# Performance work log

Hardware: AMD Instinct MI355X
Metric: run time of the kernel (lower is better)

## Reference

```python
import jax, jax.numpy as jnp
import numpy as np


def _conv(x, w, b, stride=1, pad=0):
    # x: NCHW, w: OIHW (torch layout)
    y = jax.lax.conv_general_dilated(
        x, w, (stride, stride), [(pad, pad), (pad, pad)],
        dimension_numbers=('NCHW', 'OIHW', 'NCHW'))
    return y + b[None, :, None, None]


def _convT(x, w, b):
    # torch ConvTranspose2d(k=4, stride=2, padding=1); w: [Cin, Cout, 4, 4]
    wf = jnp.flip(w, (2, 3)).transpose(1, 0, 2, 3)  # -> OIHW
    y = jax.lax.conv_general_dilated(
        x, wf, (1, 1), [(2, 2), (2, 2)], lhs_dilation=(2, 2),
        dimension_numbers=('NCHW', 'OIHW', 'NCHW'))
    return y + b[None, :, None, None]


def _quantize(z, embed):
    # z: [B,H,W,D], embed: [D,K]  (eval-mode _Quantize: no EMA update)
    f = z.reshape(-1, z.shape[-1])
    dist = (f * f).sum(1, keepdims=True) - 2.0 * (f @ embed) + (embed * embed).sum(0, keepdims=True)
    ind = jnp.argmin(dist, axis=1)
    q = embed.T[ind].reshape(z.shape)
    diff = jnp.mean((jax.lax.stop_gradient(q) - z) ** 2)[None]
    q = z + jax.lax.stop_gradient(q - z)  # straight-through
    return q, diff, ind.reshape(z.shape[:-1])


def setup_inputs() -> dict:
    key = jax.random.key(0)
    ks = jax.random.split(key, 22)
    s = 0.02
    r = lambda k, sh, sc=s: jax.random.normal(k, sh, jnp.float32) * sc
    z = lambda sh: jnp.zeros(sh, jnp.float32)
    return {
        'x': jax.random.normal(ks[0], (16, 3, 256, 256), jnp.float32),
        # encoder_bottom: two stride-2 4x4 convs, 3->128->128 (256->64)
        'wb1': r(ks[1], (128, 3, 4, 4)), 'bb1': z(128),
        'wb2': r(ks[2], (128, 128, 4, 4)), 'bb2': z(128),
        # encoder_top: one stride-2 4x4 conv, 128->128 (64->32)
        'wt1': r(ks[3], (128, 128, 4, 4)), 'bt1': z(128),
        # quantize_conv_t: 1x1, 128->64
        'wqt': r(ks[4], (64, 128, 1, 1)), 'bqt': z(64),
        'embed_t': jax.random.normal(ks[5], (64, 512), jnp.float32),
        # decoder_top: convT 64->64 (32->64)
        'wdt': r(ks[6], (64, 64, 4, 4)), 'bdt': z(64),
        # quantize_conv_b: 1x1, 192->64
        'wqb': r(ks[7], (64, 192, 1, 1)), 'bqb': z(64),
        'embed_b': jax.random.normal(ks[8], (64, 512), jnp.float32),
        # upsample_t: convT 64->64 (32->64)
        'wup': r(ks[9], (64, 64, 4, 4)), 'bup': z(64),
        # decoder_bottom: convT 128->64 (64->128), convT 64->3 (128->256)
        'wd1': r(ks[10], (128, 64, 4, 4)), 'bd1': z(64),
        'wd2': r(ks[11], (64, 3, 4, 4)), 'bd2': z(3),
    }


def reference(x, wb1, bb1, wb2, bb2, wt1, bt1, wqt, bqt, embed_t,
              wdt, bdt, wqb, bqb, embed_b, wup, bup, wd1, bd1, wd2, bd2):
    # ----- encode -----
    enc_b = jax.nn.relu(_conv(x, wb1, bb1, stride=2, pad=1))          # [B,128,128,128]
    enc_b = jax.nn.relu(_conv(enc_b, wb2, bb2, stride=2, pad=1))      # [B,128,64,64]
    enc_t = jax.nn.relu(_conv(enc_b, wt1, bt1, stride=2, pad=1))      # [B,128,32,32]

    qt = _conv(enc_t, wqt, bqt).transpose(0, 2, 3, 1)                 # [B,32,32,64]
    quant_t, diff_t, id_t = _quantize(qt, embed_t)
    quant_t = quant_t.transpose(0, 3, 1, 2)                           # [B,64,32,32]

    dec_t = _convT(quant_t, wdt, bdt)                                 # [B,64,64,64]
    enc_cat = jnp.concatenate([dec_t, enc_b], axis=1)                 # [B,192,64,64]

    qb = _conv(enc_cat, wqb, bqb).transpose(0, 2, 3, 1)               # [B,64,64,64]
    quant_b, diff_b, id_b = _quantize(qb, embed_b)
    quant_b = quant_b.transpose(0, 3, 1, 2)                           # [B,64,64,64]

    loss_commit = diff_t + diff_b                                     # [1]

    # ----- decode -----
    up_t = _convT(quant_t, wup, bup)                                  # [B,64,64,64]
    quant = jnp.concatenate([up_t, quant_b], axis=1)                  # [B,128,64,64]
    h = jax.nn.relu(_convT(quant, wd1, bd1))                          # [B,64,128,128]
    x_hat = _convT(h, wd2, bd2)                                       # [B,3,256,256]

    return x_hat, quant_t, quant_b, loss_commit, id_t, id_b
```

## Files before the change

kernel.cpp:

```cpp
#include <hip/hip_runtime.h>

#define TPB 256

typedef __attribute__((ext_vector_type(4))) float f32x4;
typedef __attribute__((ext_vector_type(8))) short bf16x8;

__global__ void wtrans_kernel(const float* __restrict__ src, float* __restrict__ dst,
                              int CIN, int COUT, int taps, int iohw) {
    int idx = blockIdx.x * TPB + threadIdx.x;
    int tot = CIN * COUT * taps;
    if (idx >= tot) return;
    int co = idx % COUT;
    int ci = (idx / COUT) % CIN;
    int tap = idx / (COUT * CIN);
    float v = iohw ? src[(ci * COUT + co) * taps + tap]
                   : src[(co * CIN + ci) * taps + tap];
    dst[idx] = v;
}

__device__ __forceinline__ unsigned bf16_rne(float v) {
    unsigned u = __float_as_uint(v);
    return (u + 0x7FFFu + ((u >> 16) & 1u)) >> 16;
}

__global__ void wtrans_bf16_kernel(const float* __restrict__ src, short* __restrict__ dst,
                                   int CIN, int COUT, int taps, int iohw, int PL) {
    int idx = blockIdx.x * TPB + threadIdx.x;
    int tot = CIN * COUT * taps;
    if (idx >= tot) return;
    int ci = idx % CIN;
    int co = (idx / CIN) % COUT;
    int tap = idx / (CIN * COUT);
    float v = iohw ? src[(ci * COUT + co) * taps + tap]
                   : src[(co * CIN + ci) * taps + tap];
    unsigned h = bf16_rne(v);
    float rem = v - __uint_as_float(h << 16);
    dst[idx] = (short)h;
    dst[idx + PL] = (short)bf16_rne(rem);
}

__global__ void wtrans_wd2_kernel(const float* __restrict__ src, short* __restrict__ dst) {
    int idx = blockIdx.x * TPB + threadIdx.x;
    if (idx >= 16384) return;
    int ci  = idx & 63;
    int co  = (idx >> 6) & 15;
    int tap = (idx >> 10) & 3;
    int cls = idx >> 12;
    int py = cls >> 1, px = cls & 1;
    int jj = tap >> 1, ii = tap & 1;
    int ky = (1 - py) + 2 * jj;
    int kx = (1 - px) + 2 * ii;
    float v = (co < 3) ? src[(ci * 3 + co) * 16 + ky * 4 + kx] : 0.f;
    dst[idx] = (short)bf16_rne(v);
}

__global__ void etrans_kernel(const float* __restrict__ et, const float* __restrict__ eb,
                              short* __restrict__ ETt, short* __restrict__ ETb) {
    int idx = blockIdx.x * TPB + threadIdx.x;
    if (idx >= 65536) return;
    const float* src = (idx < 32768) ? et : eb;
    short* dst = (idx < 32768) ? ETt : ETb;
    int i = idx & 32767;
    int k = i & 63;
    int n = i >> 6;
    float v = src[k * 512 + n];
    unsigned h = bf16_rne(v);
    float rem = v - __uint_as_float(h << 16);
    dst[i] = (short)h;
    dst[i + 32768] = (short)bf16_rne(rem);
}

__device__ __forceinline__ void cvt_split2(float a, float b, unsigned& hw, unsigned& lw) {
    unsigned ha = bf16_rne(a), hb = bf16_rne(b);
    float ra = a - __uint_as_float(ha << 16);
    float rb = b - __uint_as_float(hb << 16);
    hw = ha | (hb << 16);
    lw = bf16_rne(ra) | (bf16_rne(rb) << 16);
}
__device__ __forceinline__ unsigned cvt_pk(float a, float b) {
    return bf16_rne(a) | (bf16_rne(b) << 16);
}

template<int MODE, int CIN, int COUT, int SPLIT, int RELU,
         int IH, int IW, int OH, int OW, int R, int INBF, int OUTB, int KR>
__global__ __launch_bounds__(256) void mfma_conv(
    const void* __restrict__ inv, const short* __restrict__ Wb,
    const float* __restrict__ bias, float* __restrict__ outp,
    short* __restrict__ outb) {
    constexpr int TAPS = (MODE == 0) ? 16 : (MODE == 1 ? 4 : 1);
    constexpr int CW = (MODE == 1) ? OW / 2 : OW;
    constexpr int CH = (MODE == 1) ? OH / 2 : OH;
    constexpr int NRND = CIN / KR;
    constexpr int KC = KR / 32;
    constexpr int ST = KR + 8;
    constexpr int MTc = (COUT == 128) ? 4 : 2;
    constexpr long PLW = (long)TAPS * COUT * CIN;
    constexpr long APL_IN  = 16L * IH * IW * CIN;
    constexpr long APL_OUT = 16L * OH * OW * COUT;
    constexpr int NU4A = KR / 16;
    constexpr int TPR  = 256 / COUT;
    constexpr int SPT  = KR / TPR;
    constexpr int NU4B = SPT / 8;

    __shared__ short Ah[128 * ST];
    __shared__ short Al[SPLIT ? 128 * ST : 8];
    __shared__ short Bh[COUT * ST];
    __shared__ short Bl[SPLIT ? COUT * ST : 8];

    int bx = blockIdx.x;
    int ry = 0, rx = 0;
    if (MODE == 1) { int c = bx & 3; ry = c >> 1; rx = c & 1; bx >>= 2; }
    const int y0 = (bx % (CH / R)) * R;
    const int n  = bx / (CH / R);

    const int tid = threadIdx.x;
    const int p   = tid >> 1;
    const int akb = (tid & 1) * (KR / 2);
    const int rr = p / CW, xx = p % CW;
    const int bco = tid / TPR;
    const int bk  = (tid % TPR) * SPT;
    const int lane = tid & 63, wv = tid >> 6;
    const int quad = lane >> 4, l16 = lane & 15;
    const int mbase = (COUT == 128) ? (wv & 1) * 64 : wv * 32;
    const int nbase = (COUT == 128) ? (wv >> 1) * 64 : 0;

    f32x4 acc[MTc][4];
#pragma unroll
    for (int mt = 0; mt < MTc; ++mt)
#pragma unroll
        for (int nt = 0; nt < 4; ++nt) acc[mt][nt] = f32x4{0.f, 0.f, 0.f, 0.f};

#pragma unroll 1
    for (int tap = 0; tap < TAPS; ++tap) {
        int iy, ix, wt;
        if (MODE == 0) {
            int ky = tap >> 2, kx = tap & 3;
            iy = 2 * (y0 + rr) - 1 + ky;
            ix = 2 * xx - 1 + kx;
            wt = tap;
        } else if (MODE == 1) {
            int jj = tap >> 1, ii = tap & 1;
            iy = (y0 + rr) + ry - jj;
            ix = xx + rx - ii;
            wt = ((1 - ry) + 2 * jj) * 4 + ((1 - rx) + 2 * ii);
        } else {
            iy = y0 + rr; ix = xx; wt = 0;
        }
        const bool av = (MODE == 2) ||
                        ((iy >= 0) && (iy < IH) && (ix >= 0) && (ix < IW));
        const long abase = ((long)(n * IH + iy) * IW + ix) * CIN + akb;

#pragma unroll 1
        for (int ko = 0; ko < NRND; ++ko) {
            __syncthreads();
            if constexpr (INBF) {
                const short* sb = (const short*)inv + abase + ko * KR;
#pragma unroll
                for (int u = 0; u < NU4A; ++u) {
                    uint4 h = av ? *(const uint4*)(sb + 8 * u) : make_uint4(0, 0, 0, 0);
                    *(uint4*)&Ah[p * ST + akb + 8 * u] = h;
                }
                if constexpr (SPLIT) {
#pragma unroll
                    for (int u = 0; u < NU4A; ++u) {
                        uint4 l = av ? *(const uint4*)(sb + APL_IN + 8 * u) : make_uint4(0, 0, 0, 0);
                        *(uint4*)&Al[p * ST + akb + 8 * u] = l;
                    }
                }
            } else {
                const float* sp = (const float*)inv + abase + ko * KR;
#pragma unroll
                for (int u = 0; u < NU4A; ++u) {
                    float4 f0, f1;
                    if (av) { f0 = *(const float4*)(sp + 8 * u); f1 = *(const float4*)(sp + 8 * u + 4); }
                    else { f0.x=f0.y=f0.z=f0.w=0.f; f1 = f0; }
                    unsigned h0, l0, h1, l1, h2, l2, h3, l3;
                    cvt_split2(f0.x, f0.y, h0, l0); cvt_split2(f0.z, f0.w, h1, l1);
                    cvt_split2(f1.x, f1.y, h2, l2); cvt_split2(f1.z, f1.w, h3, l3);
                    *(uint4*)&Ah[p * ST + akb + 8 * u] = make_uint4(h0, h1, h2, h3);
                    if constexpr (SPLIT)
                        *(uint4*)&Al[p * ST + akb + 8 * u] = make_uint4(l0, l1, l2, l3);
                }
            }
            {
                const short* wr = Wb + ((long)wt * COUT + bco) * CIN + ko * KR + bk;
#pragma unroll
                for (int u = 0; u < NU4B; ++u) {
                    *(uint4*)&Bh[bco * ST + bk + 8 * u] = *(const uint4*)(wr + 8 * u);
                    if constexpr (SPLIT)
                        *(uint4*)&Bl[bco * ST + bk + 8 * u] = *(const uint4*)(wr + PLW + 8 * u);
                }
            }
            __syncthreads();
#pragma unroll
            for (int kc = 0; kc < KC; ++kc) {
                bf16x8 ahf[MTc], alf[SPLIT ? MTc : 1];
#pragma unroll
                for (int mt = 0; mt < MTc; ++mt) {
                    ahf[mt] = *(const bf16x8*)&Ah[(mbase + mt * 16 + l16) * ST + kc * 32 + quad * 8];
                    if constexpr (SPLIT)
                        alf[mt] = *(const bf16x8*)&Al[(mbase + mt * 16 + l16) * ST + kc * 32 + quad * 8];
                }
#pragma unroll
                for (int nt = 0; nt < 4; ++nt) {
                    bf16x8 bhf = *(const bf16x8*)&Bh[(nbase + nt * 16 + l16) * ST + kc * 32 + quad * 8];
#pragma unroll
                    for (int mt = 0; mt < MTc; ++mt)
                        acc[mt][nt] = __builtin_amdgcn_mfma_f32_16x16x32_bf16(ahf[mt], bhf, acc[mt][nt], 0, 0, 0);
                    if constexpr (SPLIT) {
                        bf16x8 blf = *(const bf16x8*)&Bl[(nbase + nt * 16 + l16) * ST + kc * 32 + quad * 8];
#pragma unroll
                        for (int mt = 0; mt < MTc; ++mt) {
                            acc[mt][nt] = __builtin_amdgcn_mfma_f32_16x16x32_bf16(alf[mt], bhf, acc[mt][nt], 0, 0, 0);
                            acc[mt][nt] = __builtin_amdgcn_mfma_f32_16x16x32_bf16(ahf[mt], blf, acc[mt][nt], 0, 0, 0);
                        }
                    }
                }
            }
        }
    }
#pragma unroll
    for (int mt = 0; mt < MTc; ++mt)
#pragma unroll
        for (int nt = 0; nt < 4; ++nt) {
            int co = nbase + nt * 16 + l16;
            float bv = bias[co];
#pragma unroll
            for (int r = 0; r < 4; ++r) {
                int pl = mbase + mt * 16 + quad * 4 + r;
                int rr2 = pl / CW, x2 = pl % CW;
                int oy, ox;
                if (MODE == 1) { oy = 2 * (y0 + rr2) + ry; ox = 2 * x2 + rx; }
                else           { oy = y0 + rr2; ox = x2; }
                float vv = acc[mt][nt][r] + bv;
                if (RELU) vv = fmaxf(vv, 0.f);
                long oidx = ((long)(n * OH + oy) * OW + ox) * COUT + co;
                if constexpr (OUTB == 0) outp[oidx] = vv;
                if constexpr (OUTB == 3) {
                    unsigned hh = bf16_rne(vv);
                    outb[oidx] = (short)hh;
                    outb[oidx + APL_OUT] = (short)bf16_rne(vv - __uint_as_float(hh << 16));
                }
                if constexpr (OUTB == 2) outb[oidx] = (short)bf16_rne(vv);
            }
        }
}

template<int MODE, int CIN, int COUT, int BM, int RELU, int IH, int IW, int OH, int OW>
__global__ __launch_bounds__(256) void conv_gemm(
    const float* __restrict__ in, const float* __restrict__ Wt,
    const float* __restrict__ bias, float* __restrict__ out) {
    constexpr int CHUNK  = 64;
    constexpr int NCH    = CIN / CHUNK;
    constexpr int CO_PER = (COUT == 128) ? 4 : 2;
    constexpr int PX_PER = BM / 8;
    constexpr int TAPS   = (MODE == 0) ? 16 : (MODE == 1 ? 4 : 1);
    __shared__ float As[CHUNK * BM];
    __shared__ float Bs[CHUNK * COUT];
    const int tid = threadIdx.x;
    const int bx  = blockIdx.x;
    int n, oy, ox0 = 0, par = 0;
    if (MODE == 1) {
        par = bx & 1;
        oy  = (bx >> 1) % OH;
        n   = bx / (2 * OH);
    } else {
        constexpr int SPR = OW / BM;
        int s = bx % SPR;
        oy = (bx / SPR) % OH;
        n  = bx / (SPR * OH);
        ox0 = s * BM;
    }
    const int cog = tid & 31;
    const int pxg = tid >> 5;
    const int co0 = cog * CO_PER, px0 = pxg * PX_PER;
    float acc[PX_PER][CO_PER];
#pragma unroll
    for (int q = 0; q < PX_PER; ++q)
#pragma unroll
        for (int j = 0; j < CO_PER; ++j) acc[q][j] = 0.f;
    constexpr int TPX  = 256 / BM;
    constexpr int CIPT = CHUNK / TPX;
    const int spx  = tid / TPX;
    const int sci0 = (tid % TPX) * CIPT;
    const int py   = oy & 1;

#pragma unroll 1
    for (int tap = 0; tap < TAPS; ++tap) {
        int iy, twi, sx;
        if (MODE == 0) {
            int ky = tap >> 2, kx = tap & 3;
            iy  = 2 * oy - 1 + ky;
            sx  = 2 * (ox0 + spx) - 1 + kx;
            twi = tap;
        } else if (MODE == 1) {
            int jj = tap >> 1, ii = tap & 1;
            iy  = ((oy + 1) >> 1) - jj;
            sx  = spx + par - ii;
            twi = ((1 - py) + 2 * jj) * 4 + ((1 - par) + 2 * ii);
        } else {
            iy = oy; sx = ox0 + spx; twi = 0;
        }
        const bool pxv = (iy >= 0) && (iy < IH) && (sx >= 0) && (sx < IW);
        const float* srcp = in + (((long)n * IH + iy) * IW + sx) * CIN + sci0;
#pragma unroll 1
        for (int cb = 0; cb < NCH; ++cb) {
            __syncthreads();
            float4 tmp[CIPT / 4];
#pragma unroll
            for (int t4 = 0; t4 < CIPT / 4; ++t4) {
                if (pxv) tmp[t4] = *(const float4*)(srcp + cb * CHUNK + 4 * t4);
                else { tmp[t4].x = 0.f; tmp[t4].y = 0.f; tmp[t4].z = 0.f; tmp[t4].w = 0.f; }
            }
#pragma unroll
            for (int t4 = 0; t4 < CIPT / 4; ++t4) {
                As[(sci0 + 4 * t4 + 0) * BM + spx] = tmp[t4].x;
                As[(sci0 + 4 * t4 + 1) * BM + spx] = tmp[t4].y;
                As[(sci0 + 4 * t4 + 2) * BM + spx] = tmp[t4].z;
                As[(sci0 + 4 * t4 + 3) * BM + spx] = tmp[t4].w;
            }
            {
                const float4* wsrc = (const float4*)(Wt + ((long)twi * CIN + cb * CHUNK) * COUT);
#pragma unroll
                for (int t4 = 0; t4 < (CHUNK * COUT) / 1024; ++t4)
                    ((float4*)Bs)[tid + 256 * t4] = wsrc[tid + 256 * t4];
            }
            __syncthreads();
#pragma unroll 4
            for (int k = 0; k < CHUNK; ++k) {
                float a[PX_PER];
#pragma unroll
                for (int t4 = 0; t4 < PX_PER / 4; ++t4)
                    *(float4*)&a[4 * t4] = *(const float4*)&As[k * BM + px0 + 4 * t4];
                if constexpr (CO_PER == 4) {
                    float4 b = *(const float4*)&Bs[k * COUT + co0];
#pragma unroll
                    for (int q = 0; q < PX_PER; ++q) {
                        acc[q][0] = fmaf(a[q], b.x, acc[q][0]);
                        acc[q][1] = fmaf(a[q], b.y, acc[q][1]);
                        acc[q][2] = fmaf(a[q], b.z, acc[q][2]);
                        acc[q][3] = fmaf(a[q], b.w, acc[q][3]);
                    }
                } else {
                    float2 b = *(const float2*)&Bs[k * COUT + co0];
#pragma unroll
                    for (int q = 0; q < PX_PER; ++q) {
                        acc[q][0] = fmaf(a[q], b.x, acc[q][0]);
                        acc[q][1] = fmaf(a[q], b.y, acc[q][1]);
                    }
                }
            }
        }
    }
    float bv[CO_PER];
#pragma unroll
    for (int j = 0; j < CO_PER; ++j) bv[j] = bias[co0 + j];
#pragma unroll
    for (int q = 0; q < PX_PER; ++q) {
        int ox = (MODE == 1) ? (par + 2 * (px0 + q)) : (ox0 + px0 + q);
        float* op = out + (((long)n * OH + oy) * OW + ox) * COUT + co0;
        if constexpr (CO_PER == 4) {
            float4 v;
            v.x = acc[q][0] + bv[0]; v.y = acc[q][1] + bv[1];
            v.z = acc[q][2] + bv[2]; v.w = acc[q][3] + bv[3];
            if (RELU) { v.x = fmaxf(v.x, 0.f); v.y = fmaxf(v.y, 0.f);
                        v.z = fmaxf(v.z, 0.f); v.w = fmaxf(v.w, 0.f); }
            *(float4*)op = v;
        } else {
            float2 v;
            v.x = acc[q][0] + bv[0]; v.y = acc[q][1] + bv[1];
            if (RELU) { v.x = fmaxf(v.x, 0.f); v.y = fmaxf(v.y, 0.f); }
            *(float2*)op = v;
        }
    }
}

__global__ __launch_bounds__(256) void convt_final_mfma(
    const short* __restrict__ h, const short* __restrict__ Wc,
    const float* __restrict__ bias, float* __restrict__ out) {
    const int HW = 128;
    __shared__ short HB[3 * 130 * 72];
    __shared__ float Sout[6 * 260];

    const int tid = threadIdx.x;
    const int y = blockIdx.x & 127;
    const int n = blockIdx.x >> 7;
    const int lane = tid & 63, wv = tid >> 6;
    const int quad = lane >> 4, l16 = lane & 15;

    for (int u = tid; u < 780; u += TPB) {
        int row = u >> 1, half = u & 1;
        int hr = row / 130, xc = row % 130;
        int hy = y - 1 + hr, hx = xc - 1;
        bool ok = (hy >= 0 && hy < HW && hx >= 0 && hx < HW);
        const short* sp = h + ((long)(n * HW + hy) * HW + hx) * 64 + half * 32;
        uint4 a0, a1, a2, a3;
        if (ok) {
            a0 = *(const uint4*)sp;        a1 = *(const uint4*)(sp + 8);
            a2 = *(const uint4*)(sp + 16); a3 = *(const uint4*)(sp + 24);
        } else {
            a0 = make_uint4(0,0,0,0); a1 = a0; a2 = a0; a3 = a0;
        }
        short* dp = &HB[row * 72 + half * 32];
        *(uint4*)dp = a0; *(uint4*)(dp + 8) = a1;
        *(uint4*)(dp + 16) = a2; *(uint4*)(dp + 24) = a3;
    }
    __syncthreads();

#pragma unroll 1
    for (int cls = 0; cls < 4; ++cls) {
        const int py = cls >> 1, px = cls & 1;
        bf16x8 Bf[4][2];
#pragma unroll
        for (int tap = 0; tap < 4; ++tap)
#pragma unroll
            for (int cb = 0; cb < 2; ++cb)
                Bf[tap][cb] = *(const bf16x8*)&Wc[((cls * 4 + tap) * 16 + l16) * 64 + cb * 32 + quad * 8];

        f32x4 acc2[2] = { f32x4{0.f,0.f,0.f,0.f}, f32x4{0.f,0.f,0.f,0.f} };
#pragma unroll
        for (int mt = 0; mt < 2; ++mt) {
            const int xp0 = wv * 32 + mt * 16;
#pragma unroll
            for (int tap = 0; tap < 4; ++tap) {
                const int jj = tap >> 1, ii = tap & 1;
                const int hr = py - jj + 1;
                const int rbase = (hr * 130 + xp0 + l16 + px - ii + 1) * 72;
#pragma unroll
                for (int cb = 0; cb < 2; ++cb) {
                    bf16x8 Af = *(const bf16x8*)&HB[rbase + cb * 32 + quad * 8];
                    acc2[mt] = __builtin_amdgcn_mfma_f32_16x16x32_bf16(Af, Bf[tap][cb], acc2[mt], 0, 0, 0);
                }
            }
        }
        if (l16 < 3) {
#pragma unroll
            for (int mt = 0; mt < 2; ++mt)
#pragma unroll
                for (int r = 0; r < 4; ++r) {
                    int xp = wv * 32 + mt * 16 + quad * 4 + r;
                    Sout[(py * 3 + l16) * 260 + 2 * xp + px] = acc2[mt][r];
                }
        }
    }
    __syncthreads();

    for (int u = tid; u < 384; u += TPB) {
        int idx = u * 4;
        int rowi = idx >> 8;
        int xq   = idx & 255;
        int py = rowi / 3, co = rowi % 3;
        float bv = bias[co];
        float4 v = *(const float4*)&Sout[rowi * 260 + xq];
        v.x += bv; v.y += bv; v.z += bv; v.w += bv;
        *(float4*)&out[(((long)(n * 3 + co) * 256) + 2 * y + py) * 256 + xq] = v;
    }
}

__global__ __launch_bounds__(256) void conv1_kernel(
    const float* __restrict__ x, const float* __restrict__ Wt,
    const float* __restrict__ bias, short* __restrict__ outb) {
    const int IH = 256, IW = 256, OH = 128, OW = 128, BM = 64;
    const long APL0 = 16L * 128 * 128 * 128;
    int bx = blockIdx.x;
    int sx = bx & 1;
    int oy = (bx >> 1) & 127;
    int n  = bx >> 8;
    int ox0 = sx * BM;
    __shared__ float Bs[16 * 3 * 128];
    __shared__ float Ts[3 * 4 * 132];
    int tid = threadIdx.x;
    for (int i = tid; i < 6144 / 4; i += TPB)
        ((float4*)Bs)[i] = ((const float4*)Wt)[i];
    int iy0 = 2 * oy - 1;
    for (int idx = tid; idx < 3 * 4 * 130; idx += TPB) {
        int ci = idx / 520; int r = idx % 520;
        int ky = r / 130;   int xx = r % 130;
        int iy = iy0 + ky;  int ix = 2 * ox0 - 1 + xx;
        float v = 0.f;
        if (iy >= 0 && iy < IH && ix >= 0 && ix < IW)
            v = x[((n * 3 + ci) * IH + iy) * IW + ix];
        Ts[(ci * 4 + ky) * 132 + xx] = v;
    }
    __syncthreads();
    int cog = tid & 31, pxg = tid >> 5;
    int co0 = cog * 4, px0 = pxg * 8;
    float acc[8][4];
#pragma unroll
    for (int i = 0; i < 8; ++i)
#pragma unroll
        for (int j = 0; j < 4; ++j) acc[i][j] = 0.f;
#pragma unroll 1
    for (int ky = 0; ky < 4; ++ky)
#pragma unroll 1
        for (int kx = 0; kx < 4; ++kx)
#pragma unroll
            for (int ci = 0; ci < 3; ++ci) {
                float4 b = *(const float4*)&Bs[((ky * 4 + kx) * 3 + ci) * 128 + co0];
                const float* trow = &Ts[(ci * 4 + ky) * 132 + kx];
#pragma unroll
                for (int q = 0; q < 8; ++q) {
                    float a = trow[2 * (px0 + q)];
                    acc[q][0] = fmaf(a, b.x, acc[q][0]);
                    acc[q][1] = fmaf(a, b.y, acc[q][1]);
                    acc[q][2] = fmaf(a, b.z, acc[q][2]);
                    acc[q][3] = fmaf(a, b.w, acc[q][3]);
                }
            }
    float4 bb = *(const float4*)&bias[co0];
#pragma unroll
    for (int q = 0; q < 8; ++q) {
        int ox = ox0 + px0 + q;
        float v0 = fmaxf(acc[q][0] + bb.x, 0.f);
        float v1 = fmaxf(acc[q][1] + bb.y, 0.f);
        float v2 = fmaxf(acc[q][2] + bb.z, 0.f);
        float v3 = fmaxf(acc[q][3] + bb.w, 0.f);
        unsigned h0, l0, h1, l1;
        cvt_split2(v0, v1, h0, l0);
        cvt_split2(v2, v3, h1, l1);
        long pix = ((long)n * OH + oy) * OW + ox;
        *(uint2*)&outb[pix * 128 + co0]        = make_uint2(h0, h1);
        *(uint2*)&outb[APL0 + pix * 128 + co0] = make_uint2(l0, l1);
    }
}

__global__ void enorm_kernel(const float* __restrict__ et, const float* __restrict__ eb,
                             float* __restrict__ nt, float* __restrict__ nb) {
    int k = blockIdx.x * TPB + threadIdx.x;
    if (k >= 1024) return;
    const float* e = (k < 512) ? et : eb;
    float* o = (k < 512) ? nt : nb;
    int kk = k & 511;
    float s = 0.f;
#pragma unroll 8
    for (int d = 0; d < 64; ++d) { float v = e[d * 512 + kk]; s = fmaf(v, v, s); }
    o[kk] = s;
}

__global__ __launch_bounds__(256) void quantize_mfma(
    const float* __restrict__ f, const short* __restrict__ ET,
    const float* __restrict__ embed, const float* __restrict__ enorm,
    float* __restrict__ qn, short* __restrict__ qnb, float* __restrict__ qc,
    float* __restrict__ ido, float* __restrict__ dsum, int M, int HW) {
    __shared__ short Fh[64 * 72];
    __shared__ short Fl[64 * 72];
    __shared__ float S[64 * 65];
    __shared__ int   KI[64];
    __shared__ float wsum[4];

    const int tid = threadIdx.x;
    const int lane = tid & 63, wv = tid >> 6;
    const int quad = lane >> 4, l16 = lane & 15;
    const int R0 = blockIdx.x * 64;

    {
        int row = tid >> 2;
        int k0 = (tid & 3) * 16;
        const float* sp = f + (long)(R0 + row) * 64 + k0;
        unsigned hw[8], lw[8];
#pragma unroll
        for (int i = 0; i < 4; ++i) {
            float4 p = *(const float4*)(sp + 4 * i);
            cvt_split2(p.x, p.y, hw[2 * i], lw[2 * i]);
            cvt_split2(p.z, p.w, hw[2 * i + 1], lw[2 * i + 1]);
        }
        short* dh = &Fh[row * 72 + k0];
        short* dl = &Fl[row * 72 + k0];
        *(uint4*)(dh)     = make_uint4(hw[0], hw[1], hw[2], hw[3]);
        *(uint4*)(dh + 8) = make_uint4(hw[4], hw[5], hw[6], hw[7]);
        *(uint4*)(dl)     = make_uint4(lw[0], lw[1], lw[2], lw[3]);
        *(uint4*)(dl + 8) = make_uint4(lw[4], lw[5], lw[6], lw[7]);
    }
    __syncthreads();

    const int arow = (wv * 16 + l16) * 72;
    bf16x8 Ah0 = *(const bf16x8*)&Fh[arow + quad * 8];
    bf16x8 Ah1 = *(const bf16x8*)&Fh[arow + 32 + quad * 8];
    bf16x8 Al0 = *(const bf16x8*)&Fl[arow + quad * 8];
    bf16x8 Al1 = *(const bf16x8*)&Fl[arow + 32 + quad * 8];

    float bestv[4];
    int   besti[4];
#pragma unroll
    for (int r = 0; r < 4; ++r) { bestv[r] = 3.4e38f; besti[r] = 0; }

    const short* ETlo = ET + 32768;
#pragma unroll 2
    for (int j = 0; j < 32; ++j) {
        const int nb = (j * 16 + l16) * 64 + quad * 8;
        bf16x8 Bh0 = *(const bf16x8*)(ET + nb);
        bf16x8 Bh1 = *(const bf16x8*)(ET + nb + 32);
        bf16x8 Bl0 = *(const bf16x8*)(ETlo + nb);
        bf16x8 Bl1 = *(const bf16x8*)(ETlo + nb + 32);
        f32x4 acc = f32x4{0.f, 0.f, 0.f, 0.f};
        acc = __builtin_amdgcn_mfma_f32_16x16x32_bf16(Ah0, Bh0, acc, 0, 0, 0);
        acc = __builtin_amdgcn_mfma_f32_16x16x32_bf16(Ah1, Bh1, acc, 0, 0, 0);
        acc = __builtin_amdgcn_mfma_f32_16x16x32_bf16(Al0, Bh0, acc, 0, 0, 0);
        acc = __builtin_amdgcn_mfma_f32_16x16x32_bf16(Al1, Bh1, acc, 0, 0, 0);
        acc = __builtin_amdgcn_mfma_f32_16x16x32_bf16(Ah0, Bl0, acc, 0, 0, 0);
        acc = __builtin_amdgcn_mfma_f32_16x16x32_bf16(Ah1, Bl1, acc, 0, 0, 0);
        float en = enorm[j * 16 + l16];
        int   ni = j * 16 + l16;
#pragma unroll
        for (int r = 0; r < 4; ++r) {
            float s = fmaf(-2.f, acc[r], en);
            if (s < bestv[r]) { bestv[r] = s; besti[r] = ni; }
        }
    }
#pragma unroll
    for (int m = 1; m < 16; m <<= 1) {
#pragma unroll
        for (int r = 0; r < 4; ++r) {
            float ov = __shfl_xor(bestv[r], m);
            int   oi = __shfl_xor(besti[r], m);
            if (ov < bestv[r] || (ov == bestv[r] && oi < besti[r])) {
                bestv[r] = ov; besti[r] = oi;
            }
        }
    }
    if (l16 == 0) {
#pragma unroll
        for (int r = 0; r < 4; ++r) KI[wv * 16 + quad * 4 + r] = besti[r];
    }
    __syncthreads();

    float ddacc = 0.f;
#pragma unroll 1
    for (int r16 = 0; r16 < 16; ++r16) {
        int row = wv * 16 + r16;
        int k = KI[row];
        float ev = embed[lane * 512 + k];
        float fv = f[(long)(R0 + row) * 64 + lane];
        long qi = (long)(R0 + row) * 64 + lane;
        qn[qi] = ev;
        qnb[qi] = (short)bf16_rne(ev);
        S[row * 65 + lane] = ev;
        float dq = ev - fv;
        ddacc = fmaf(dq, dq, ddacc);
        if (lane == 0) ido[R0 + row] = (float)k;
    }
#pragma unroll
    for (int off = 1; off < 64; off <<= 1) ddacc += __shfl_xor(ddacc, off);
    if (lane == 0) wsum[wv] = ddacc;
    __syncthreads();
    if (tid == 0)
        atomicAdd(dsum, wsum[0] + wsum[1] + wsum[2] + wsum[3]);

    int nn = R0 / HW;
    int rem0 = R0 - nn * HW;
    int px = tid & 63;
    int cg = tid >> 6;
#pragma unroll
    for (int it = 0; it < 16; ++it) {
        int c = cg + 4 * it;
        qc[((long)nn * 64 + c) * HW + rem0 + px] = S[px * 65 + c];
    }
}

__global__ void concat_rec_kernel(const float* __restrict__ a, const short* __restrict__ bh,
                                  float* __restrict__ o, int M) {
    const long PLB = 8388608L;
    int idx = blockIdx.x * TPB + threadIdx.x;
    if (idx >= M * 48) return;
    int row = idx / 48;
    int c4  = (idx - row * 48) * 4;
    float4 v;
    if (c4 < 64) v = *(const float4*)(a + (long)row * 64 + c4);
    else {
        int cc = c4 - 64;
        uint2 h = *(const uint2*)(bh + (long)row * 128 + cc);
        uint2 l = *(const uint2*)(bh + PLB + (long)row * 128 + cc);
        v.x = __uint_as_float(h.x << 16)         + __uint_as_float(l.x << 16);
        v.y = __uint_as_float(h.x & 0xFFFF0000u) + __uint_as_float(l.x & 0xFFFF0000u);
        v.z = __uint_as_float(h.y << 16)         + __uint_as_float(l.y << 16);
        v.w = __uint_as_float(h.y & 0xFFFF0000u) + __uint_as_float(l.y & 0xFFFF0000u);
    }
    *(float4*)(o + (long)row * 192 + c4) = v;
}

__global__ void concat_qcat_kernel(const float* __restrict__ a, const short* __restrict__ qh,
                                   short* __restrict__ o, int M) {
    int idx = blockIdx.x * TPB + threadIdx.x;
    if (idx >= M * 32) return;
    int row = idx / 32;
    int c4  = (idx - row * 32) * 4;
    uint2 w;
    if (c4 < 64) {
        float4 v = *(const float4*)(a + (long)row * 64 + c4);
        w = make_uint2(cvt_pk(v.x, v.y), cvt_pk(v.z, v.w));
    } else {
        w = *(const uint2*)(qh + (long)row * 64 + (c4 - 64));
    }
    *(uint2*)(o + (long)row * 128 + c4) = w;
}

__global__ void loss_kernel(const float* __restrict__ sums, float* __restrict__ out) {
    out[0] = sums[0] * (1.f / (16384.f * 64.f)) + sums[1] * (1.f / (65536.f * 64.f));
}

extern "C" void kernel_launch(void* const* d_in, const int* in_sizes, int n_in,
                              void* d_out, int out_size, void* d_ws, size_t ws_size,
                              hipStream_t stream) {
    const float* x   = (const float*)d_in[0];
    const float* wb1 = (const float*)d_in[1];  const float* bb1 = (const float*)d_in[2];
    const float* wb2 = (const float*)d_in[3];  const float* bb2 = (const float*)d_in[4];
    const float* wt1 = (const float*)d_in[5];  const float* bt1 = (const float*)d_in[6];
    const float* wqt = (const float*)d_in[7];  const float* bqt = (const float*)d_in[8];
    const float* embed_t = (const float*)d_in[9];
    const float* wdt = (const float*)d_in[10]; const float* bdt = (const float*)d_in[11];
    const float* wqb = (const float*)d_in[12]; const float* bqb = (const float*)d_in[13];
    const float* embed_b = (const float*)d_in[14];
    const float* wup = (const float*)d_in[15]; const float* bup = (const float*)d_in[16];
    const float* wd1 = (const float*)d_in[17]; const float* bd1 = (const float*)d_in[18];
    const float* wd2 = (const float*)d_in[19]; const float* bd2 = (const float*)d_in[20];
    float* out = (float*)d_out;
    float* ws  = (float*)d_ws;

    float* O_XHAT = out;
    float* O_QT   = out + 3145728;
    float* O_QB   = out + 4194304;
    float* O_LOSS = out + 8388608;
    float* O_IDT  = out + 8388609;
    float* O_IDB  = out + 8404993;

    float* W_WB1  = ws + 0;
    short* WB_WD2 = (short*)(ws + 16384);
    short* ET_T   = (short*)(ws + 32768);
    short* ET_B   = (short*)(ws + 65536);
    short* WB_WQT = (short*)(ws + 98304);
    float* W_WDT  = ws + 540672;
    float* W_WQB  = ws + 606208;
    float* EN_T  = ws + 818176;
    float* EN_B  = ws + 818688;
    float* SUMS  = ws + 819200;
    short* T1B   = (short*)(ws + 1048576);
    const long BIG = 9437184;
    short* T0B   = (short*)(ws + BIG);
    short* T2B   = (short*)(ws + BIG);
    float* QT    = ws + BIG + 2097152;
    float* QTN   = ws + BIG + 3145728;
    short* QTNB  = (short*)(ws + BIG + 4194304);
    float* DECT  = ws + BIG + 4718592;
    float* ECAT  = ws + BIG + 8912896;
    float* QB    = ws + BIG + 21495808;
    short* QBNB  = (short*)(ws + BIG + 25690112);
    float* QND   = ws + BIG + 27787264;
    float* UPT   = ws + BIG + 4718592;
    short* QCATB = (short*)(ws + BIG + 8912896);
    short* HBUFB = (short*)(ws + BIG + 16777216);
    short* WB_BF2 = (short*)(ws + 42991616);
    short* WB_BT1 = (short*)(ws + 43253760);
    short* WB_BD1 = (short*)(ws + 43515904);
    short* WB_BUP = (short*)(ws + 43646976);

    auto wt_launch = [&](const float* src, float* dst, int cin, int cout, int taps, int iohw) {
        int tot = cin * cout * taps;
        wtrans_kernel<<<(tot + TPB - 1) / TPB, TPB, 0, stream>>>(src, dst, cin, cout, taps, iohw);
    };
    auto wtb_launch = [&](const float* src, short* dst, int cin, int cout, int taps, int iohw) {
        int tot = cin * cout * taps;
        wtrans_bf16_kernel<<<(tot + TPB - 1) / TPB, TPB, 0, stream>>>(src, dst, cin, cout, taps, iohw, tot);
    };
    wt_launch(wb1, W_WB1, 3, 128, 16, 0);
    wt_launch(wdt, W_WDT, 64, 64, 16, 1);
    wt_launch(wqb, W_WQB, 192, 64, 1, 0);
    wtrans_wd2_kernel<<<64, TPB, 0, stream>>>(wd2, WB_WD2);
    wtb_launch(wb2, WB_BF2, 128, 128, 16, 0);
    wtb_launch(wt1, WB_BT1, 128, 128, 16, 0);
    wtb_launch(wqt, WB_WQT, 128, 64, 1, 0);
    wtb_launch(wd1, WB_BD1, 128, 64, 16, 1);
    wtb_launch(wup, WB_BUP, 64, 64, 16, 1);
    enorm_kernel<<<4, TPB, 0, stream>>>(embed_t, embed_b, EN_T, EN_B);
    etrans_kernel<<<256, TPB, 0, stream>>>(embed_t, embed_b, ET_T, ET_B);
    hipError_t e0 = hipMemsetAsync((void*)SUMS, 0, 2 * sizeof(float), stream);
    (void)e0;

    conv1_kernel<<<4096, TPB, 0, stream>>>(x, W_WB1, bb1, T0B);
    mfma_conv<0, 128, 128, 1, 1, 128, 128, 64, 64, 2, 1, 3, 32>
        <<<512, TPB, 0, stream>>>(T0B, WB_BF2, bb2, nullptr, T1B);
    mfma_conv<0, 128, 128, 1, 1, 64, 64, 32, 32, 4, 1, 3, 32>
        <<<128, TPB, 0, stream>>>(T1B, WB_BT1, bt1, nullptr, T2B);
    mfma_conv<2, 128, 64, 1, 0, 32, 32, 32, 32, 4, 1, 0, 64>
        <<<128, TPB, 0, stream>>>(T2B, WB_WQT, bqt, QT, nullptr);
    quantize_mfma<<<256, TPB, 0, stream>>>(QT, ET_T, embed_t, EN_T, QTN, QTNB,
                                           O_QT, O_IDT, SUMS, 16384, 1024);
    conv_gemm<1, 64, 64, 32, 0, 32, 32, 64, 64><<<2048, TPB, 0, stream>>>(QTN, W_WDT, bdt, DECT);
    concat_rec_kernel<<<12288, TPB, 0, stream>>>(DECT, T1B, ECAT, 65536);
    conv_gemm<2, 192, 64, 64, 0, 64, 64, 64, 64><<<1024, TPB, 0, stream>>>(ECAT, W_WQB, bqb, QB);
    quantize_mfma<<<1024, TPB, 0, stream>>>(QB, ET_B, embed_b, EN_B, QND, QBNB,
                                            O_QB, O_IDB, SUMS + 1, 65536, 4096);
    mfma_conv<1, 64, 64, 0, 0, 32, 32, 64, 64, 4, 1, 0, 64>
        <<<512, TPB, 0, stream>>>(QTNB, WB_BUP, bup, UPT, nullptr);
    concat_qcat_kernel<<<8192, TPB, 0, stream>>>(UPT, QBNB, QCATB, 65536);
    mfma_conv<1, 128, 64, 0, 1, 64, 64, 128, 128, 2, 1, 2, 64>
        <<<2048, TPB, 0, stream>>>(QCATB, WB_BD1, bd1, nullptr, HBUFB);
    convt_final_mfma<<<2048, TPB, 0, stream>>>(HBUFB, WB_WD2, bd2, O_XHAT);
    loss_kernel<<<1, 1, 0, stream>>>(SUMS, O_LOSS);

    (void)in_sizes; (void)n_in; (void)out_size; (void)ws_size;
}
```

Before: 730.6 us.

## Split output channels across blocks and XOR-swizzle LDS tiles in mfma_conv

Adds an NSP template parameter that splits the 128 output channels of the two stride-2 encoder convs across two blocks, doubling the grid (512→1024, 128→256) to improve CU occupancy. It also replaces the padded row-major LDS indexing with an XOR swizzle of 8-element groups within each 32-wide k chunk, meant to reduce bank conflicts on MFMA fragment loads. The channel split halves per-block MFMA work but makes each A tile get loaded and split-converted twice, adding global traffic and redundant staging.

Result: slower. 817.3 us (+11.9%).

```diff
diff --git a/kernel.cpp b/kernel.cpp
--- a/kernel.cpp
+++ b/kernel.cpp
@@ -81,8 +81,16 @@
     return bf16_rne(a) | (bf16_rne(b) << 16);
 }
 
+template<int ST>
+__device__ __forceinline__ int lidx(int row, int koff) {
+    int g  = (koff >> 3) & 3;
+    int kc = koff & ~31;
+    int gs = g ^ ((row >> 3) & 3);
+    return row * ST + kc + (gs << 3);
+}
+
 template<int MODE, int CIN, int COUT, int SPLIT, int RELU,
-         int IH, int IW, int OH, int OW, int R, int INBF, int OUTB, int KR>
+         int IH, int IW, int OH, int OW, int R, int INBF, int OUTB, int KR, int NSP>
 __global__ __launch_bounds__(256) void mfma_conv(
     const void* __restrict__ inv, const short* __restrict__ Wb,
     const float* __restrict__ bias, float* __restrict__ outp,
@@ -90,24 +98,27 @@
     constexpr int TAPS = (MODE == 0) ? 16 : (MODE == 1 ? 4 : 1);
     constexpr int CW = (MODE == 1) ? OW / 2 : OW;
     constexpr int CH = (MODE == 1) ? OH / 2 : OH;
+    constexpr int NCOUT = COUT / NSP;
     constexpr int NRND = CIN / KR;
     constexpr int KC = KR / 32;
     constexpr int ST = KR + 8;
-    constexpr int MTc = (COUT == 128) ? 4 : 2;
+    constexpr int MTc = (NCOUT == 128) ? 4 : 2;
     constexpr long PLW = (long)TAPS * COUT * CIN;
     constexpr long APL_IN  = 16L * IH * IW * CIN;
     constexpr long APL_OUT = 16L * OH * OW * COUT;
     constexpr int NU4A = KR / 16;
-    constexpr int TPR  = 256 / COUT;
+    constexpr int TPR  = 256 / NCOUT;
     constexpr int SPT  = KR / TPR;
     constexpr int NU4B = SPT / 8;
 
     __shared__ short Ah[128 * ST];
     __shared__ short Al[SPLIT ? 128 * ST : 8];
-    __shared__ short Bh[COUT * ST];
-    __shared__ short Bl[SPLIT ? COUT * ST : 8];
+    __shared__ short Bh[NCOUT * ST];
+    __shared__ short Bl[SPLIT ? NCOUT * ST : 8];
 
     int bx = blockIdx.x;
+    int co_off = 0;
+    if (NSP == 2) { co_off = (bx & 1) * NCOUT; bx >>= 1; }
     int ry = 0, rx = 0;
     if (MODE == 1) { int c = bx & 3; ry = c >> 1; rx = c & 1; bx >>= 2; }
     const int y0 = (bx % (CH / R)) * R;
@@ -121,8 +132,8 @@
     const int bk  = (tid % TPR) * SPT;
     const int lane = tid & 63, wv = tid >> 6;
     const int quad = lane >> 4, l16 = lane & 15;
-    const int mbase = (COUT == 128) ? (wv & 1) * 64 : wv * 32;
-    const int nbase = (COUT == 128) ? (wv >> 1) * 64 : 0;
+    const int mbase = (NCOUT == 128) ? (wv & 1) * 64 : wv * 32;
+    const int nbase = (NCOUT == 128) ? (wv >> 1) * 64 : 0;
 
     f32x4 acc[MTc][4];
 #pragma unroll
@@ -158,13 +169,13 @@
 #pragma unroll
                 for (int u = 0; u < NU4A; ++u) {
                     uint4 h = av ? *(const uint4*)(sb + 8 * u) : make_uint4(0, 0, 0, 0);
-                    *(uint4*)&Ah[p * ST + akb + 8 * u] = h;
+                    *(uint4*)&Ah[lidx<ST>(p, akb + 8 * u)] = h;
                 }
                 if constexpr (SPLIT) {
 #pragma unroll
                     for (int u = 0; u < NU4A; ++u) {
                         uint4 l = av ? *(const uint4*)(sb + APL_IN + 8 * u) : make_uint4(0, 0, 0, 0);
-                        *(uint4*)&Al[p * ST + akb + 8 * u] = l;
+                        *(uint4*)&Al[lidx<ST>(p, akb + 8 * u)] = l;
                     }
                 }
             } else {
@@ -177,18 +188,18 @@
                     unsigned h0, l0, h1, l1, h2, l2, h3, l3;
                     cvt_split2(f0.x, f0.y, h0, l0); cvt_split2(f0.z, f0.w, h1, l1);
                     cvt_split2(f1.x, f1.y, h2, l2); cvt_split2(f1.z, f1.w, h3, l3);
-                    *(uint4*)&Ah[p * ST + akb + 8 * u] = make_uint4(h0, h1, h2, h3);
+                    *(uint4*)&Ah[lidx<ST>(p, akb + 8 * u)] = make_uint4(h0, h1, h2, h3);
                     if constexpr (SPLIT)
-                        *(uint4*)&Al[p * ST + akb + 8 * u] = make_uint4(l0, l1, l2, l3);
+                        *(uint4*)&Al[lidx<ST>(p, akb + 8 * u)] = make_uint4(l0, l1, l2, l3);
                 }
             }
             {
-                const short* wr = Wb + ((long)wt * COUT + bco) * CIN + ko * KR + bk;
+                const short* wr = Wb + ((long)wt * COUT + co_off + bco) * CIN + ko * KR + bk;
 #pragma unroll
                 for (int u = 0; u < NU4B; ++u) {
-                    *(uint4*)&Bh[bco * ST + bk + 8 * u] = *(const uint4*)(wr + 8 * u);
+                    *(uint4*)&Bh[lidx<ST>(bco, bk + 8 * u)] = *(const uint4*)(wr + 8 * u);
                     if constexpr (SPLIT)
-                        *(uint4*)&Bl[bco * ST + bk + 8 * u] = *(const uint4*)(wr + PLW + 8 * u);
+                        *(uint4*)&Bl[lidx<ST>(bco, bk + 8 * u)] = *(const uint4*)(wr + PLW + 8 * u);
                 }
             }
             __syncthreads();
@@ -197,18 +208,20 @@
                 bf16x8 ahf[MTc], alf[SPLIT ? MTc : 1];
 #pragma unroll
                 for (int mt = 0; mt < MTc; ++mt) {
-                    ahf[mt] = *(const bf16x8*)&Ah[(mbase + mt * 16 + l16) * ST + kc * 32 + quad * 8];
+                    int mrow = mbase + mt * 16 + l16;
+                    ahf[mt] = *(const bf16x8*)&Ah[lidx<ST>(mrow, kc * 32 + quad * 8)];
                     if constexpr (SPLIT)
-                        alf[mt] = *(const bf16x8*)&Al[(mbase + mt * 16 + l16) * ST + kc * 32 + quad * 8];
+                        alf[mt] = *(const bf16x8*)&Al[lidx<ST>(mrow, kc * 32 + quad * 8)];
                 }
 #pragma unroll
                 for (int nt = 0; nt < 4; ++nt) {
-                    bf16x8 bhf = *(const bf16x8*)&Bh[(nbase + nt * 16 + l16) * ST + kc * 32 + quad * 8];
+                    int nrow = nbase + nt * 16 + l16;
+                    bf16x8 bhf = *(const bf16x8*)&Bh[lidx<ST>(nrow, kc * 32 + quad * 8)];
 #pragma unroll
                     for (int mt = 0; mt < MTc; ++mt)
                         acc[mt][nt] = __builtin_amdgcn_mfma_f32_16x16x32_bf16(ahf[mt], bhf, acc[mt][nt], 0, 0, 0);
                     if constexpr (SPLIT) {
-                        bf16x8 blf = *(const bf16x8*)&Bl[(nbase + nt * 16 + l16) * ST + kc * 32 + quad * 8];
+                        bf16x8 blf = *(const bf16x8*)&Bl[lidx<ST>(nrow, kc * 32 + quad * 8)];
 #pragma unroll
                         for (int mt = 0; mt < MTc; ++mt) {
                             acc[mt][nt] = __builtin_amdgcn_mfma_f32_16x16x32_bf16(alf[mt], bhf, acc[mt][nt], 0, 0, 0);
@@ -223,7 +236,7 @@
     for (int mt = 0; mt < MTc; ++mt)
 #pragma unroll
         for (int nt = 0; nt < 4; ++nt) {
-            int co = nbase + nt * 16 + l16;
+            int co = co_off + nbase + nt * 16 + l16;
             float bv = bias[co];
 #pragma unroll
             for (int r = 0; r < 4; ++r) {
@@ -776,11 +789,11 @@
     (void)e0;
 
     conv1_kernel<<<4096, TPB, 0, stream>>>(x, W_WB1, bb1, T0B);
-    mfma_conv<0, 128, 128, 1, 1, 128, 128, 64, 64, 2, 1, 3, 32>
-        <<<512, TPB, 0, stream>>>(T0B, WB_BF2, bb2, nullptr, T1B);
-    mfma_conv<0, 128, 128, 1, 1, 64, 64, 32, 32, 4, 1, 3, 32>
-        <<<128, TPB, 0, stream>>>(T1B, WB_BT1, bt1, nullptr, T2B);
-    mfma_conv<2, 128, 64, 1, 0, 32, 32, 32, 32, 4, 1, 0, 64>
+    mfma_conv<0, 128, 128, 1, 1, 128, 128, 64, 64, 2, 1, 3, 32, 2>
+        <<<1024, TPB, 0, stream>>>(T0B, WB_BF2, bb2, nullptr, T1B);
+    mfma_conv<0, 128, 128, 1, 1, 64, 64, 32, 32, 4, 1, 3, 32, 2>
+        <<<256, TPB, 0, stream>>>(T1B, WB_BT1, bt1, nullptr, T2B);
+    mfma_conv<2, 128, 64, 1, 0, 32, 32, 32, 32, 4, 1, 0, 64, 1>
         <<<128, TPB, 0, stream>>>(T2B, WB_WQT, bqt, QT, nullptr);
     quantize_mfma<<<256, TPB, 0, stream>>>(QT, ET_T, embed_t, EN_T, QTN, QTNB,
                                            O_QT, O_IDT, SUMS, 16384, 1024);
@@ -789,10 +802,10 @@
     conv_gemm<2, 192, 64, 64, 0, 64, 64, 64, 64><<<1024, TPB, 0, stream>>>(ECAT, W_WQB, bqb, QB);
     quantize_mfma<<<1024, TPB, 0, stream>>>(QB, ET_B, embed_b, EN_B, QND, QBNB,
                                             O_QB, O_IDB, SUMS + 1, 65536, 4096);
-    mfma_conv<1, 64, 64, 0, 0, 32, 32, 64, 64, 4, 1, 0, 64>
+    mfma_conv<1, 64, 64, 0, 0, 32, 32, 64, 64, 4, 1, 0, 64, 1>
         <<<512, TPB, 0, stream>>>(QTNB, WB_BUP, bup, UPT, nullptr);
     concat_qcat_kernel<<<8192, TPB, 0, stream>>>(UPT, QBNB, QCATB, 65536);
-    mfma_conv<1, 128, 64, 0, 1, 64, 64, 128, 128, 2, 1, 2, 64>
+    mfma_conv<1, 128, 64, 0, 1, 64, 64, 128, 128, 2, 1, 2, 64, 1>
         <<<2048, TPB, 0, stream>>>(QCATB, WB_BD1, bd1, nullptr, HBUFB);
     convt_final_mfma<<<2048, TPB, 0, stream>>>(HBUFB, WB_WD2, bd2, O_XHAT);
     loss_kernel<<<1, 1, 0, stream>>>(SUMS, O_LOSS);
```
